# Kernel optimization log

Measured on AMD Instinct MI355X. Metric: run time of the kernel, lower is better.

## Reference

```python
import jax, jax.numpy as jnp
import numpy as np

ALPHA = 0.5  # LeakyReLU negative slope


def setup_inputs() -> dict:
    key = jax.random.key(0)
    k1, k2, k3, k4, k5 = jax.random.split(key, 5)
    B, N, S, SO, K = 16, 2048, 12, 12, 32
    return {
        "fushed_features": jax.random.normal(k1, (B, N, 64), dtype=jnp.float32),
        "input_data": jax.random.normal(k2, (B, N, S), dtype=jnp.float32),
        "W": jax.random.normal(k3, (S, SO), dtype=jnp.float32) * (1.414 / np.sqrt(S)),
        "a": jax.random.normal(k4, (2 * SO, 1), dtype=jnp.float32) * 0.3,
        "idx": jax.random.randint(k5, (B, N, K), 0, N, dtype=jnp.int32),
    }


def reference(fushed_features, input_data, W, a, idx):
    # input_data: (B, N, S); W: (S, SO); a: (2*SO, 1); idx: (B, N, K)
    B, N, S = input_data.shape
    SO = W.shape[1]
    wh = input_data @ W  # (B, N, SO)
    # concat([wh_i, wh_j]) @ a  ==  wh_i @ a[:SO] + wh_j @ a[SO:]  (exact same math,
    # avoids materializing the (B,N,N,2*SO) concat the torch code builds)
    e_src = wh @ a[:SO, 0]  # (B, N)
    e_dst = wh @ a[SO:, 0]  # (B, N)
    scores = jax.nn.leaky_relu(e_src[:, :, None] + e_dst[:, None, :], negative_slope=ALPHA)  # (B,N,N)
    att = jnp.take_along_axis(scores, idx, axis=2)  # (B, N, K) gather top-k neighbor scores
    att = jax.nn.softmax(att, axis=-1)  # softmax over the K neighbors
    # gather neighbor time series: (B, N, K, S)
    neigh = input_data[jnp.arange(B)[:, None, None], idx]
    out = att[..., None] * neigh  # (B, N, K, S)
    return out
```

## Files before the change

kernel.cpp:

```cpp
#include <hip/hip_runtime.h>


#define GAT_N 2048
#define GAT_ALPHA 0.5f
#define PPB 8

__global__ __launch_bounds__(256) void gat_fused(
    const float* __restrict__ x,
    const float* __restrict__ W,
    const float* __restrict__ a,
    const int*   __restrict__ idx,
    float*       __restrict__ out)
{
    __shared__ float wvec[24];
    __shared__ float stage[PPB * 384];
    const int tid = threadIdx.x;

    if (tid < 24) {
        const int s = tid % 12;
        const float* av = a + (tid < 12 ? 0 : 12);
        float acc = 0.f;
        #pragma unroll
        for (int t = 0; t < 12; ++t) acc += W[s * 12 + t] * av[t];
        wvec[tid] = acc;
    }
    __syncthreads();

    const int p    = tid >> 5;
    const int pair = blockIdx.x * PPB + p;
    const int k    = tid & 31;

    const float4* rowi = (const float4*)(x + (size_t)pair * 12);
    const float4 i0 = rowi[0], i1 = rowi[1], i2 = rowi[2];
    const float e_src =
        i0.x*wvec[0] + i0.y*wvec[1] + i0.z*wvec[2]  + i0.w*wvec[3] +
        i1.x*wvec[4] + i1.y*wvec[5] + i1.z*wvec[6]  + i1.w*wvec[7] +
        i2.x*wvec[8] + i2.y*wvec[9] + i2.z*wvec[10] + i2.w*wvec[11];

    const int j   = idx[(size_t)pair * 32 + k];
    const int nbr = (pair & ~(GAT_N - 1)) + j;
    const float4* rowj = (const float4*)(x + (size_t)nbr * 12);
    const float4 n0 = rowj[0], n1 = rowj[1], n2 = rowj[2];
    const float e_dst =
        n0.x*wvec[12] + n0.y*wvec[13] + n0.z*wvec[14] + n0.w*wvec[15] +
        n1.x*wvec[16] + n1.y*wvec[17] + n1.z*wvec[18] + n1.w*wvec[19] +
        n2.x*wvec[20] + n2.y*wvec[21] + n2.z*wvec[22] + n2.w*wvec[23];

    float sc = e_src + e_dst;
    sc = sc > 0.f ? sc : GAT_ALPHA * sc;
    float m = sc;
    #pragma unroll
    for (int off = 16; off; off >>= 1) m = fmaxf(m, __shfl_xor(m, off, 32));
    const float ex = __expf(sc - m);
    float sum = ex;
    #pragma unroll
    for (int off = 16; off; off >>= 1) sum += __shfl_xor(sum, off, 32);
    const float att = ex / sum;

    float4* st = (float4*)(stage + p * 384 + k * 12);
    st[0] = make_float4(att * n0.x, att * n0.y, att * n0.z, att * n0.w);
    st[1] = make_float4(att * n1.x, att * n1.y, att * n1.z, att * n1.w);
    st[2] = make_float4(att * n2.x, att * n2.y, att * n2.z, att * n2.w);
    __syncthreads();

    const float4* sm4 = (const float4*)stage;
    float4* o4 = (float4*)(out + (size_t)blockIdx.x * PPB * 384);
    #pragma unroll
    for (int r = 0; r < 3; ++r) o4[tid + 256 * r] = sm4[tid + 256 * r];
}

extern "C" void kernel_launch(void* const* d_in, const int* in_sizes, int n_in,
                              void* d_out, int out_size, void* d_ws, size_t ws_size,
                              hipStream_t stream) {
    const float* x   = (const float*)d_in[1];
    const float* W   = (const float*)d_in[2];
    const float* a   = (const float*)d_in[3];
    const int*   idx = (const int*)d_in[4];
    float* out = (float*)d_out;

    const int pairs  = in_sizes[1] / 12;
    const int blocks = pairs / PPB;
    gat_fused<<<blocks, 256, 0, stream>>>(x, W, a, idx, out);
}
```

Baseline: 88.12 us.

## Split into precompute kernel with padded rows and cached attention logits

Adds a precompute kernel that computes per-node source and destination attention logits once and writes x padded to 16-float rows in workspace. The main kernel then gathers each neighbor from a 64-byte aligned row plus one scalar instead of recomputing two 12-term dot products per pair. This removes redundant dot-product work and makes gathers line-aligned, at the cost of an extra launch and extra workspace traffic. It falls back to the fused kernel if the workspace is too small.

New measurement: 90.55 us. +2.8%, slower.

```diff
diff --git a/kernel.cpp b/kernel.cpp
--- a/kernel.cpp
+++ b/kernel.cpp
@@ -5,12 +5,102 @@
 #define GAT_ALPHA 0.5f
 #define PPB 8
 
-__global__ __launch_bounds__(256) void gat_fused(
+__global__ __launch_bounds__(256) void gat_precomp(
     const float* __restrict__ x,
     const float* __restrict__ W,
     const float* __restrict__ a,
+    float*       __restrict__ xp,
+    float*       __restrict__ es,
+    float*       __restrict__ ed)
+{
+    __shared__ float wvec[24];
+    __shared__ float rows[256 * 12];
+    const int tid = threadIdx.x;
+
+    if (tid < 24) {
+        const int s = tid % 12;
+        const float* av = a + (tid < 12 ? 0 : 12);
+        float acc = 0.f;
+        #pragma unroll
+        for (int t = 0; t < 12; ++t) acc += W[s * 12 + t] * av[t];
+        wvec[tid] = acc;
+    }
+    const float4* g4 = (const float4*)(x + (size_t)blockIdx.x * 256 * 12);
+    float4* l4 = (float4*)rows;
+    #pragma unroll
+    for (int r = 0; r < 3; ++r) l4[tid + 256 * r] = g4[tid + 256 * r];
+    __syncthreads();
+
+    const int n = blockIdx.x * 256 + tid;
+    const float* row = rows + tid * 12;
+    float s0 = 0.f, s1 = 0.f;
+    #pragma unroll
+    for (int t = 0; t < 12; ++t) {
+        s0 += row[t] * wvec[t];
+        s1 += row[t] * wvec[12 + t];
+    }
+    es[n] = s0;
+    ed[n] = s1;
+
+    float4* o4 = (float4*)(xp + (size_t)blockIdx.x * 256 * 16);
+    #pragma unroll
+    for (int c = 0; c < 4; ++c) {
+        const int g  = tid + 256 * c;
+        const int r  = g >> 2;
+        const int pc = g & 3;
+        float4 v = make_float4(0.f, 0.f, 0.f, 0.f);
+        if (pc < 3) v = *(const float4*)(rows + r * 12 + pc * 4);
+        o4[g] = v;
+    }
+}
+
+__global__ __launch_bounds__(256) void gat_main(
+    const float* __restrict__ xp,
+    const float* __restrict__ es_arr,
+    const float* __restrict__ ed_arr,
     const int*   __restrict__ idx,
     float*       __restrict__ out)
+{
+    __shared__ float stage[PPB * 384];
+    const int tid  = threadIdx.x;
+    const int p    = tid >> 5;
+    const int pair = blockIdx.x * PPB + p;
+    const int k    = tid & 31;
+
+    const int j   = idx[(size_t)pair * 32 + k];
+    const int nbr = (pair & ~(GAT_N - 1)) + j;
+
+    const float4* rowj = (const float4*)(xp + (size_t)nbr * 16);
+    const float4 n0 = rowj[0], n1 = rowj[1], n2 = rowj[2];
+
+    const float e  = es_arr[pair] + ed_arr[nbr];
+    float sc = e > 0.f ? e : GAT_ALPHA * e;
+
+    float m = sc;
+    #pragma unroll
+    for (int off = 16; off; off >>= 1) m = fmaxf(m, __shfl_xor(m, off, 32));
+    const float ex = __expf(sc - m);
+    float sum = ex;
+    #pragma unroll
+    for (int off = 16; off; off >>= 1) sum += __shfl_xor(sum, off, 32);
+    const float att = ex / sum;
+
+    float4* st = (float4*)(stage + p * 384 + k * 12);
+    st[0] = make_float4(att * n0.x, att * n0.y, att * n0.z, att * n0.w);
+    st[1] = make_float4(att * n1.x, att * n1.y, att * n1.z, att * n1.w);
+    st[2] = make_float4(att * n2.x, att * n2.y, att * n2.z, att * n2.w);
+    __syncthreads();
+
+    const float4* sm4 = (const float4*)stage;
+    float4* o4 = (float4*)(out + (size_t)blockIdx.x * PPB * 384);
+    #pragma unroll
+    for (int r = 0; r < 3; ++r) o4[tid + 256 * r] = sm4[tid + 256 * r];
+}
+
+__global__ __launch_bounds__(256) void gat_fused(
+    const float* __restrict__ x, const float* __restrict__ W,
+    const float* __restrict__ a, const int* __restrict__ idx,
+    float* __restrict__ out)
 {
     __shared__ float wvec[24];
     __shared__ float stage[PPB * 384];
@@ -80,5 +170,16 @@
 
     const int pairs  = in_sizes[1] / 12;
     const int blocks = pairs / PPB;
-    gat_fused<<<blocks, 256, 0, stream>>>(x, W, a, idx, out);
+
+    const size_t xp_bytes = (size_t)pairs * 16 * sizeof(float);
+    const size_t e_bytes  = (size_t)pairs * sizeof(float);
+    if (ws_size >= xp_bytes + 2 * e_bytes) {
+        float* xp = (float*)d_ws;
+        float* es = xp + (size_t)pairs * 16;
+        float* ed = es + pairs;
+        gat_precomp<<<pairs / 256, 256, 0, stream>>>(x, W, a, xp, es, ed);
+        gat_main<<<blocks, 256, 0, stream>>>(xp, es, ed, idx, out);
+    } else {
+        gat_fused<<<blocks, 256, 0, stream>>>(x, W, a, idx, out);
+    }
 }
```

## Stage whole batch rows in LDS and precompute per-node dst scores

Applied to the files above, without the earlier changes.

Adds a kernel that loads one batch's full x (2048x12 floats) into shared memory and precomputes e_dst for every node and e_src for its 128 rows. Neighbour gathers then read from LDS instead of global memory. The softmax drops the max-reduction and clamps the exponent instead, and output is written directly with coalesced float4 stores. Each block redundantly loads the full batch slab (16 blocks per batch) and uses about 100KB of LDS with 1024 threads, which limits occupancy to one block per CU.

After: 85.54 us. 2.9% less time.

```diff
diff --git a/kernel.cpp b/kernel.cpp
--- a/kernel.cpp
+++ b/kernel.cpp
@@ -3,17 +3,109 @@
 
 #define GAT_N 2048
 #define GAT_ALPHA 0.5f
-#define PPB 8
+#define PPBLK 128
+#define THREADS 1024
 
-__global__ __launch_bounds__(256) void gat_fused(
+__global__ __launch_bounds__(THREADS, 1) void gat_lds(
     const float* __restrict__ x,
     const float* __restrict__ W,
     const float* __restrict__ a,
     const int*   __restrict__ idx,
     float*       __restrict__ out)
 {
+    __shared__ float rows[GAT_N * 12];
+    __shared__ float edt[GAT_N];
+    __shared__ float es_loc[PPBLK];
     __shared__ float wvec[24];
-    __shared__ float stage[PPB * 384];
+
+    const int tid   = threadIdx.x;
+    const int b     = blockIdx.x >> 4;
+    const int blk16 = blockIdx.x & 15;
+
+    if (tid < 24) {
+        const int s = tid % 12;
+        const float* av = a + (tid < 12 ? 0 : 12);
+        float acc = 0.f;
+        #pragma unroll
+        for (int t = 0; t < 12; ++t) acc += W[s * 12 + t] * av[t];
+        wvec[tid] = acc;
+    }
+
+    {
+        const float4* g4 = (const float4*)(x + (size_t)b * GAT_N * 12);
+        float4* l4 = (float4*)rows;
+        #pragma unroll
+        for (int r = 0; r < 6; ++r) l4[tid + THREADS * r] = g4[tid + THREADS * r];
+    }
+    __syncthreads();
+
+    #pragma unroll
+    for (int c = 0; c < 2; ++c) {
+        const int n = tid + THREADS * c;
+        const float* row = rows + n * 12;
+        float acc = 0.f;
+        #pragma unroll
+        for (int t = 0; t < 12; ++t) acc += row[t] * wvec[12 + t];
+        edt[n] = acc;
+    }
+    if (tid < PPBLK) {
+        const float* row = rows + (blk16 * PPBLK + tid) * 12;
+        float acc = 0.f;
+        #pragma unroll
+        for (int t = 0; t < 12; ++t) acc += row[t] * wvec[t];
+        es_loc[tid] = acc;
+    }
+    __syncthreads();
+
+    const int slot = tid >> 5;
+    const int k    = tid & 31;
+    const int pairG0 = (b << 11) + blk16 * PPBLK + slot;
+
+    int jv[4];
+    #pragma unroll
+    for (int t = 0; t < 4; ++t)
+        jv[t] = idx[(size_t)(pairG0 + 32 * t) * 32 + k];
+
+    float ex[4], sum[4];
+    #pragma unroll
+    for (int t = 0; t < 4; ++t) {
+        float e = es_loc[slot + 32 * t] + edt[jv[t]];
+        e = e > 0.f ? e : GAT_ALPHA * e;
+        ex[t] = __expf(fminf(e, 80.f));
+        sum[t] = ex[t];
+    }
+    #pragma unroll
+    for (int off = 16; off; off >>= 1) {
+        #pragma unroll
+        for (int t = 0; t < 4; ++t) sum[t] += __shfl_xor(sum[t], off, 32);
+    }
+    float att[4];
+    #pragma unroll
+    for (int t = 0; t < 4; ++t) att[t] = ex[t] / sum[t];
+
+    #pragma unroll
+    for (int t = 0; t < 4; ++t) {
+        float4* o4 = (float4*)out + (size_t)(pairG0 + 32 * t) * 96;
+        #pragma unroll
+        for (int r = 0; r < 3; ++r) {
+            const int f  = r * 32 + k;
+            const int kk = f / 3;
+            const int q  = f - 3 * kk;
+            const float attk = __shfl(att[t], kk, 32);
+            const int   jk   = __shfl(jv[t],  kk, 32);
+            const float4 v = *(const float4*)(rows + jk * 12 + 4 * q);
+            o4[f] = make_float4(attk * v.x, attk * v.y, attk * v.z, attk * v.w);
+        }
+    }
+}
+
+__global__ __launch_bounds__(256) void gat_fused(
+    const float* __restrict__ x, const float* __restrict__ W,
+    const float* __restrict__ a, const int* __restrict__ idx,
+    float* __restrict__ out)
+{
+    __shared__ float wvec[24];
+    __shared__ float stage[8 * 384];
     const int tid = threadIdx.x;
 
     if (tid < 24) {
@@ -27,7 +119,7 @@
     __syncthreads();
 
     const int p    = tid >> 5;
-    const int pair = blockIdx.x * PPB + p;
+    const int pair = blockIdx.x * 8 + p;
     const int k    = tid & 31;
 
     const float4* rowi = (const float4*)(x + (size_t)pair * 12);
@@ -64,7 +156,7 @@
     __syncthreads();
 
     const float4* sm4 = (const float4*)stage;
-    float4* o4 = (float4*)(out + (size_t)blockIdx.x * PPB * 384);
+    float4* o4 = (float4*)(out + (size_t)blockIdx.x * 8 * 384);
     #pragma unroll
     for (int r = 0; r < 3; ++r) o4[tid + 256 * r] = sm4[tid + 256 * r];
 }
@@ -78,7 +170,11 @@
     const int*   idx = (const int*)d_in[4];
     float* out = (float*)d_out;
 
-    const int pairs  = in_sizes[1] / 12;
-    const int blocks = pairs / PPB;
-    gat_fused<<<blocks, 256, 0, stream>>>(x, W, a, idx, out);
+    const int pairs = in_sizes[1] / 12;
+
+    if ((pairs & (GAT_N - 1)) == 0) {
+        gat_lds<<<pairs / PPBLK, THREADS, 0, stream>>>(x, W, a, idx, out);
+    } else {
+        gat_fused<<<pairs / 8, 256, 0, stream>>>(x, W, a, idx, out);
+    }
 }
```

## Add gat_hi kernel that regathers neighbor rows instead of staging scaled outputs

Applied to the files above, without the earlier changes.

A new kernel drops the 12KB shared staging buffer. It stores only per-pair attention weights and neighbor indices in shared memory and then re-reads the neighbor rows from global memory (likely cache hits) to write coalesced output. It also computes W·a per lane and broadcasts it with shuffles instead of a shared-memory prologue and barrier, and it skips the max-reduction by clamping the exponent at 80. The intent is to cut shared-memory traffic and raise occupancy, at the cost of extra global reads and a softmax that could overflow or lose accuracy if scores were large.

Result: slower. 96.03 us (+9.0%).

```diff
diff --git a/kernel.cpp b/kernel.cpp
--- a/kernel.cpp
+++ b/kernel.cpp
@@ -3,17 +3,91 @@
 
 #define GAT_N 2048
 #define GAT_ALPHA 0.5f
-#define PPB 8
 
-__global__ __launch_bounds__(256) void gat_fused(
+__global__ __launch_bounds__(256) void gat_hi(
     const float* __restrict__ x,
     const float* __restrict__ W,
     const float* __restrict__ a,
     const int*   __restrict__ idx,
     float*       __restrict__ out)
 {
+    __shared__ float att_tab[8 * 32];
+    __shared__ int   j_tab[8 * 32];
+
+    const int tid  = threadIdx.x;
+    const int slot = tid >> 5;
+    const int k    = tid & 31;
+    const int pair = blockIdx.x * 8 + slot;
+    const int base = pair & ~(GAT_N - 1);
+
+    const int j   = idx[(size_t)pair * 32 + k];
+    const int nbr = base + j;
+
+    const float4* rowj = (const float4*)(x + (size_t)nbr * 12);
+    const float4 n0 = rowj[0], n1 = rowj[1], n2 = rowj[2];
+    const float4* rowi = (const float4*)(x + (size_t)pair * 12);
+    const float4 i0 = rowi[0], i1 = rowi[1], i2 = rowi[2];
+
+    float acc;
+    {
+        const int l     = tid & 63;
+        const int id24  = l % 24;
+        const int s     = id24 % 12;
+        const float* av = a + (id24 < 12 ? 0 : 12);
+        acc = 0.f;
+        #pragma unroll
+        for (int t = 0; t < 12; ++t) acc += W[s * 12 + t] * av[t];
+    }
+    float ws[12], wd[12];
+    #pragma unroll
+    for (int s = 0; s < 12; ++s) {
+        ws[s] = __shfl(acc, s, 64);
+        wd[s] = __shfl(acc, 12 + s, 64);
+    }
+
+    const float e_src =
+        i0.x*ws[0] + i0.y*ws[1] + i0.z*ws[2]  + i0.w*ws[3] +
+        i1.x*ws[4] + i1.y*ws[5] + i1.z*ws[6]  + i1.w*ws[7] +
+        i2.x*ws[8] + i2.y*ws[9] + i2.z*ws[10] + i2.w*ws[11];
+    const float e_dst =
+        n0.x*wd[0] + n0.y*wd[1] + n0.z*wd[2]  + n0.w*wd[3] +
+        n1.x*wd[4] + n1.y*wd[5] + n1.z*wd[6]  + n1.w*wd[7] +
+        n2.x*wd[8] + n2.y*wd[9] + n2.z*wd[10] + n2.w*wd[11];
+
+    float e = e_src + e_dst;
+    e = e > 0.f ? e : GAT_ALPHA * e;
+    const float ex = __expf(fminf(e, 80.f));
+    float sum = ex;
+    #pragma unroll
+    for (int off = 16; off; off >>= 1) sum += __shfl_xor(sum, off, 32);
+    const float att = ex / sum;
+
+    att_tab[slot * 32 + k] = att;
+    j_tab[slot * 32 + k]   = j;
+    __syncthreads();
+
+    float4* o4 = (float4*)out + (size_t)blockIdx.x * 768;
+    #pragma unroll
+    for (int r = 0; r < 3; ++r) {
+        const int f   = tid + 256 * r;
+        const int pl  = f / 96;
+        const int rem = f - 96 * pl;
+        const int kk  = rem / 3;
+        const int q   = rem - 3 * kk;
+        const float attk = att_tab[pl * 32 + kk];
+        const int   jk   = j_tab[pl * 32 + kk];
+        const float4 v = *((const float4*)(x + (size_t)(base + jk) * 12) + q);
+        o4[f] = make_float4(attk * v.x, attk * v.y, attk * v.z, attk * v.w);
+    }
+}
+
+__global__ __launch_bounds__(256) void gat_fused(
+    const float* __restrict__ x, const float* __restrict__ W,
+    const float* __restrict__ a, const int* __restrict__ idx,
+    float* __restrict__ out)
+{
     __shared__ float wvec[24];
-    __shared__ float stage[PPB * 384];
+    __shared__ float stage[8 * 384];
     const int tid = threadIdx.x;
 
     if (tid < 24) {
@@ -27,7 +101,7 @@
     __syncthreads();
 
     const int p    = tid >> 5;
-    const int pair = blockIdx.x * PPB + p;
+    const int pair = blockIdx.x * 8 + p;
     const int k    = tid & 31;
 
     const float4* rowi = (const float4*)(x + (size_t)pair * 12);
@@ -64,7 +138,7 @@
     __syncthreads();
 
     const float4* sm4 = (const float4*)stage;
-    float4* o4 = (float4*)(out + (size_t)blockIdx.x * PPB * 384);
+    float4* o4 = (float4*)(out + (size_t)blockIdx.x * 8 * 384);
     #pragma unroll
     for (int r = 0; r < 3; ++r) o4[tid + 256 * r] = sm4[tid + 256 * r];
 }
@@ -78,7 +152,11 @@
     const int*   idx = (const int*)d_in[4];
     float* out = (float*)d_out;
 
-    const int pairs  = in_sizes[1] / 12;
-    const int blocks = pairs / PPB;
-    gat_fused<<<blocks, 256, 0, stream>>>(x, W, a, idx, out);
+    const int pairs = in_sizes[1] / 12;
+
+    if ((pairs & (GAT_N - 1)) == 0) {
+        gat_hi<<<pairs / 8, 256, 0, stream>>>(x, W, a, idx, out);
+    } else {
+        gat_fused<<<pairs / 8, 256, 0, stream>>>(x, W, a, idx, out);
+    }
 }
```
